# Kernel optimization log

Hardware: AMD Instinct MI355X
Metric: run time of the kernel (lower is better)

The kernel has to match this reference:

```python
import jax, jax.numpy as jnp
import numpy as np
import math

B, S, D_MODEL = 2, 2048, 1024
NUM_HEADS, D_KEY, D_VALUE = 16, 64, 64


def setup_inputs() -> dict:
    key = jax.random.key(0)
    ks = jax.random.split(key, 7)
    query = jax.random.normal(ks[0], (B, S, D_MODEL), dtype=jnp.float32)
    k_in = jax.random.normal(ks[1], (B, S, D_MODEL), dtype=jnp.float32)
    v_in = jax.random.normal(ks[2], (B, S, D_MODEL), dtype=jnp.float32)
    # boolean mask, True = masked out (masked_fill_ semantics); causal mask
    mask = jnp.triu(jnp.ones((S, S), dtype=bool), k=1)[None, None, :, :]
    scale = 1.0 / math.sqrt(D_MODEL)
    w_q = jax.random.normal(ks[3], (D_MODEL, NUM_HEADS * D_KEY), dtype=jnp.float32) * scale
    w_k = jax.random.normal(ks[4], (D_MODEL, NUM_HEADS * D_KEY), dtype=jnp.float32) * scale
    w_v = jax.random.normal(ks[5], (D_MODEL, NUM_HEADS * D_VALUE), dtype=jnp.float32) * scale
    w_o = jax.random.normal(ks[6], (NUM_HEADS * D_VALUE, D_MODEL), dtype=jnp.float32) * scale
    return {"query": query, "key": k_in, "value": v_in, "mask": mask,
            "w_q": w_q, "w_k": w_k, "w_v": w_v, "w_o": w_o}


def reference(query, key, value, mask, w_q, w_k, w_v, w_o):
    b, sq, _ = query.shape
    sk = key.shape[1]
    # projections, split heads: [B, H, S, d]
    q = (query @ w_q).reshape(b, sq, NUM_HEADS, D_KEY).transpose(0, 2, 1, 3)
    k = (key @ w_k).reshape(b, sk, NUM_HEADS, D_KEY).transpose(0, 2, 1, 3)
    v = (value @ w_v).reshape(b, sk, NUM_HEADS, D_VALUE).transpose(0, 2, 1, 3)
    # scaled scores [B, H, Sq, Sk], eager masked softmax (as in source)
    scores = jnp.einsum('bhqd,bhkd->bhqk', q, k) / math.sqrt(D_KEY)
    scores = jnp.where(mask, -jnp.inf, scores)
    attn = jax.nn.softmax(scores, axis=-1)
    # AV, merge heads, output projection (dropout is identity in eval / p=0)
    out = jnp.einsum('bhqk,bhkd->bhqd', attn, v)
    out = out.transpose(0, 2, 1, 3).reshape(b, sq, NUM_HEADS * D_VALUE)
    return out @ w_o
```

## Files before the change

### kernel.cpp

```cpp
#include <hip/hip_runtime.h>


typedef __attribute__((ext_vector_type(8))) short v8s;
typedef __attribute__((ext_vector_type(4))) float v4f;

#define MFMA16(a, b, c) __builtin_amdgcn_mfma_f32_16x16x32_bf16(a, b, c, 0, 0, 0)

#define GLOBAL_AS __attribute__((address_space(1)))
#define LDS_AS __attribute__((address_space(3)))

__device__ __forceinline__ void gload_lds16(const void* g, void* l) {
  __builtin_amdgcn_global_load_lds((const GLOBAL_AS void*)g, (LDS_AS void*)l, 16, 0, 0);
}

__device__ __forceinline__ short f2bf(float f) {
  union { float f; unsigned u; } x; x.f = f;
  unsigned r = x.u + 0x7fffu + ((x.u >> 16) & 1u);
  return (short)(r >> 16);
}

__device__ __forceinline__ unsigned cvtpk_bf16(float a, float b) {
  unsigned r;
  asm("v_cvt_pk_bf16_f32 %0, %1, %2" : "=v"(r) : "v"(a), "v"(b));
  return r;
}

__device__ __forceinline__ float exp2_hw(float x) {
  float r;
  asm("v_exp_f32 %0, %1" : "=v"(r) : "v"(x));
  return r;
}

__global__ __launch_bounds__(256) void wtrans_kernel(const float* __restrict__ w0,
                                                     const float* __restrict__ w1,
                                                     const float* __restrict__ w2,
                                                     const float* __restrict__ w3,
                                                     short* __restrict__ wtbase) {
  __shared__ __align__(16) short tile[64 * 72];
  const int NN = 1024;
  int z = blockIdx.z;
  const float* W = (z == 0) ? w0 : (z == 1) ? w1 : (z == 2) ? w2 : w3;
  short* Wt = wtbase + ((z < 3) ? ((size_t)(z + 1) << 20) : 0);
  float scale = (z == 0) ? 0.125f * 1.44269504f : 1.0f;
  int n0 = blockIdx.x * 64, k0 = blockIdx.y * 64;
  int t = threadIdx.x;
  int r = t >> 4;
  int c4 = (t & 15) * 4;
  for (int rr = r; rr < 64; rr += 16) {
    float4 f = *(const float4*)(W + (size_t)(k0 + rr) * NN + n0 + c4);
    tile[(c4 + 0) * 72 + rr] = f2bf(f.x * scale);
    tile[(c4 + 1) * 72 + rr] = f2bf(f.y * scale);
    tile[(c4 + 2) * 72 + rr] = f2bf(f.z * scale);
    tile[(c4 + 3) * 72 + rr] = f2bf(f.w * scale);
  }
  __syncthreads();
  int nr = t >> 2, kc = (t & 3) * 16;
  v8s v0 = *(const v8s*)&tile[nr * 72 + kc];
  v8s v1 = *(const v8s*)&tile[nr * 72 + kc + 8];
  *(v8s*)(Wt + (size_t)(n0 + nr) * NN + k0 + kc) = v0;
  *(v8s*)(Wt + (size_t)(n0 + nr) * NN + k0 + kc + 8) = v1;
}

__global__ __launch_bounds__(256) void cast3_kernel(const float* __restrict__ s0,
                                                    const float* __restrict__ s1,
                                                    const float* __restrict__ s2,
                                                    short* __restrict__ dst,
                                                    size_t zstride) {
  int z = blockIdx.z;
  const float* src = (z == 0) ? s0 : (z == 1) ? s1 : s2;
  short* d = dst + (size_t)z * zstride;
  int i = (blockIdx.x * 256 + threadIdx.x) * 8;
  float4 f0 = *(const float4*)(src + i);
  float4 f1 = *(const float4*)(src + i + 4);
  v8s v;
  v[0] = f2bf(f0.x); v[1] = f2bf(f0.y); v[2] = f2bf(f0.z); v[3] = f2bf(f0.w);
  v[4] = f2bf(f1.x); v[5] = f2bf(f1.y); v[6] = f2bf(f1.z); v[7] = f2bf(f1.w);
  *(v8s*)(d + i) = v;
}

template <bool OUT_F32, bool V_TRANS>
__global__ __launch_bounds__(256) void gemm2_kernel(
    const short* __restrict__ Ab, size_t sA,
    const short* __restrict__ Btb, size_t sB,
    short* __restrict__ Cb, float* __restrict__ Cf, size_t sC,
    short* __restrict__ Vt,
    int M, int N, int K) {
  __shared__ __align__(16) short As[2][128 * 32];
  __shared__ __align__(16) short Bs[2][128 * 32];

  int gx = gridDim.x, gy = gridDim.y;
  int id = blockIdx.x + gx * (blockIdx.y + gy * blockIdx.z);
  int nwg = gx * gy * gridDim.z;
  int v = (id & 7) * (nwg >> 3) + (id >> 3);
  int bx = v % gx;
  int by = (v / gx) % gy;
  int bz = v / (gx * gy);

  const short* A = Ab + (size_t)bz * sA;
  const short* Bt = Btb + (size_t)bz * sB;
  int row0 = by * 128, col0 = bx * 128;
  int t = threadIdx.x, lane = t & 63, w = t >> 6;
  int wm = (w >> 1) * 64, wn = (w & 1) * 64;
  int lr = lane & 15, lg = lane >> 4;

  v4f acc[4][4];
#pragma unroll
  for (int i = 0; i < 4; ++i)
#pragma unroll
    for (int j = 0; j < 4; ++j) acc[i][j] = {0.f, 0.f, 0.f, 0.f};

  int rl = lane >> 2, sl = lane & 3;
  int scol = ((sl ^ (rl ^ (rl >> 2))) & 3) * 8;
  const short* gA = A + (size_t)(row0 + w * 16 + rl) * K + scol;
  const short* gB = Bt + (size_t)(col0 + w * 16 + rl) * K + scol;
  const size_t rstep = (size_t)64 * K;

#define GEMM_STAGE(buf, k0_)                              \
  do {                                                    \
    gload_lds16(gA + (k0_), &As[buf][w * 512]);           \
    gload_lds16(gA + rstep + (k0_), &As[buf][(w + 4) * 512]); \
    gload_lds16(gB + (k0_), &Bs[buf][w * 512]);           \
    gload_lds16(gB + rstep + (k0_), &Bs[buf][(w + 4) * 512]); \
  } while (0)

  GEMM_STAGE(0, 0);
  __syncthreads();
  int cur = 0;
  int rsw = (lr ^ (lr >> 2)) & 3;
  for (int k0 = 0; k0 < K; k0 += 32) {
    if (k0 + 32 < K) GEMM_STAGE(cur ^ 1, k0 + 32);
    v8s af[4], bg[4];
#pragma unroll
    for (int mf = 0; mf < 4; ++mf)
      af[mf] = *(const v8s*)&As[cur][(wm + mf * 16 + lr) * 32 + ((lg ^ rsw) * 8)];
#pragma unroll
    for (int nf = 0; nf < 4; ++nf)
      bg[nf] = *(const v8s*)&Bs[cur][(wn + nf * 16 + lr) * 32 + ((lg ^ rsw) * 8)];
    __builtin_amdgcn_s_setprio(1);
#pragma unroll
    for (int mf = 0; mf < 4; ++mf)
#pragma unroll
      for (int nf = 0; nf < 4; ++nf)
        acc[mf][nf] = MFMA16(af[mf], bg[nf], acc[mf][nf]);
    __builtin_amdgcn_s_setprio(0);
    __syncthreads();
    cur ^= 1;
  }
#undef GEMM_STAGE

  if (V_TRANS && bz == 2) {
#pragma unroll
    for (int mf = 0; mf < 4; ++mf)
#pragma unroll
      for (int nf = 0; nf < 4; ++nf) {
        int col = col0 + wn + nf * 16 + lr;
        int row = row0 + wm + mf * 16 + lg * 4;
        int bh = ((row >> 11) << 4) + (col >> 6);
        int d = col & 63, s = row & 2047;
        uint2 u;
        u.x = cvtpk_bf16(acc[mf][nf][0], acc[mf][nf][1]);
        u.y = cvtpk_bf16(acc[mf][nf][2], acc[mf][nf][3]);
        *(uint2*)&Vt[((size_t)bh * 64 + d) * 2048 + s] = u;
      }
  } else {
#pragma unroll
    for (int mf = 0; mf < 4; ++mf)
#pragma unroll
      for (int nf = 0; nf < 4; ++nf)
#pragma unroll
        for (int r = 0; r < 4; ++r) {
          int row = row0 + wm + mf * 16 + lg * 4 + r;
          int col = col0 + wn + nf * 16 + lr;
          if (OUT_F32)
            (Cf + (size_t)bz * sC)[(size_t)row * N + col] = acc[mf][nf][r];
          else
            (Cb + (size_t)bz * sC)[(size_t)row * N + col] = f2bf(acc[mf][nf][r]);
        }
  }
}

__global__ __launch_bounds__(512, 4) void attn_kernel(const short* __restrict__ Qm,
                                                      const short* __restrict__ Km,
                                                      const short* __restrict__ Vt_g,
                                                      short* __restrict__ Cm) {
  const int S = 2048, DM = 1024;
  __shared__ __align__(16) short lds[21504];
  short* Ks0 = lds;
  short* Vs0 = lds + 8192;
  short* Pt = lds + 16384;
  v4f* scr = (v4f*)lds;

  int id = blockIdx.y * 16 + blockIdx.x;
  int v = (id & 7) * 64 + (id >> 3);
  int bh = v >> 4;
  int px = v & 15;
  int b = bh >> 4, h = bh & 15;
  int t = threadIdx.x, lane = t & 63, w = t >> 6;
  int g = w & 3, hh = w >> 2;
  int lr = lane & 15, lg = lane >> 4;
  size_t base = (size_t)b * S * DM + h * 64;
  size_t vbase = (size_t)bh * 64 * S;

  int srow = w * 8 + (lane >> 3);
  int scol = ((lane & 7) ^ (lane >> 3)) * 8;
  const short* gK = Km + base + (size_t)srow * DM + scol;
  const short* gV = Vt_g + vbase + (size_t)srow * S + scol;
  int sw = (lr & 7) * 8;

  const v8s vone = {0x3F80, 0x3F80, 0x3F80, 0x3F80,
                    0x3F80, 0x3F80, 0x3F80, 0x3F80};

#define ATTN_STAGE(buf, kt_)                                                  \
  do {                                                                        \
    size_t k0_ = (size_t)(kt_) * 64;                                          \
    gload_lds16(gK + k0_ * DM, &Ks0[(buf) * 4096 + w * 512]);                 \
    gload_lds16(gV + k0_, &Vs0[(buf) * 4096 + w * 512]);                      \
  } while (0)

  short* Cp = Cm + base;

#pragma unroll 1
  for (int qsel = 0; qsel < 2; ++qsel) {
    int qt = qsel ? px : (31 - px);
    int qbase = qt * 64 + g * 16;
    int qg = qbase + lr;
    int nkt = qt + 1;

    const short* Qp = Qm + base + (size_t)(qbase + lr) * DM + lg * 8;
    v8s q0 = *(const v8s*)Qp;
    v8s q1 = *(const v8s*)(Qp + 32);

    v4f o[5];
#pragma unroll
    for (int d4 = 0; d4 < 5; ++d4) o[d4] = {0.f, 0.f, 0.f, 0.f};

    ATTN_STAGE(0, 0);
    __syncthreads();
    int cur = 0;
#pragma unroll 1
    for (int kt = 0; kt < nkt; ++kt) {
      if (kt + 1 < nkt) ATTN_STAGE(cur ^ 1, kt + 1);
      int k0 = kt * 64;
      const short* Kc = &Ks0[cur * 4096];
      const short* Vc = &Vs0[cur * 4096];

      v8s ka0[2], ka1[2], vf[4];
#pragma unroll
      for (int t2 = 0; t2 < 2; ++t2) {
        int kr = hh * 32 + t2 * 16 + lr;
        ka0[t2] = *(const v8s*)&Kc[kr * 64 + ((lg * 8) ^ sw)];
        ka1[t2] = *(const v8s*)&Kc[kr * 64 + ((32 + lg * 8) ^ sw)];
      }
#pragma unroll
      for (int d4 = 0; d4 < 4; ++d4)
        vf[d4] = *(const v8s*)&Vc[(d4 * 16 + lr) * 64 + ((hh * 32 + lg * 8) ^ sw)];

      v4f st[2];
      __builtin_amdgcn_s_setprio(1);
#pragma unroll
      for (int t2 = 0; t2 < 2; ++t2) {
        v4f s = {0.f, 0.f, 0.f, 0.f};
        s = MFMA16(ka0[t2], q0, s);
        s = MFMA16(ka1[t2], q1, s);
        st[t2] = s;
      }
      __builtin_amdgcn_s_setprio(0);

      if (kt == nkt - 1) {
#pragma unroll
        for (int t2 = 0; t2 < 2; ++t2)
#pragma unroll
          for (int r = 0; r < 4; ++r)
            if (k0 + hh * 32 + t2 * 16 + lg * 4 + r > qg) st[t2][r] = -1e30f;
      }

#pragma unroll
      for (int t2 = 0; t2 < 2; ++t2) {
        uint2 u;
        u.x = cvtpk_bf16(exp2_hw(st[t2][0]), exp2_hw(st[t2][1]));
        u.y = cvtpk_bf16(exp2_hw(st[t2][2]), exp2_hw(st[t2][3]));
        *(uint2*)&Pt[w * 640 + lr * 40 + t2 * 16 + lg * 4] = u;
      }
      v8s pa = *(const v8s*)&Pt[w * 640 + lr * 40 + lg * 8];

      __builtin_amdgcn_s_setprio(1);
#pragma unroll
      for (int d4 = 0; d4 < 4; ++d4) o[d4] = MFMA16(pa, vf[d4], o[d4]);
      o[4] = MFMA16(pa, vone, o[4]);
      __builtin_amdgcn_s_setprio(0);
      __syncthreads();
      cur ^= 1;
    }

    if (hh == 1) {
#pragma unroll
      for (int d4 = 0; d4 < 5; ++d4) scr[(g * 5 + d4) * 64 + lane] = o[d4];
    }
    __syncthreads();
    if (hh == 0) {
#pragma unroll
      for (int d4 = 0; d4 < 5; ++d4) {
        v4f p = scr[(g * 5 + d4) * 64 + lane];
#pragma unroll
        for (int r = 0; r < 4; ++r) o[d4][r] += p[r];
      }
      float sv[4];
#pragma unroll
      for (int r = 0; r < 4; ++r) sv[r] = 1.0f / o[4][r];
#pragma unroll
      for (int r = 0; r < 4; ++r)
#pragma unroll
        for (int d4 = 0; d4 < 4; ++d4)
          Cp[(size_t)(qbase + lg * 4 + r) * DM + d4 * 16 + lr] =
              f2bf(o[d4][r] * sv[r]);
    }
    __syncthreads();
  }
#undef ATTN_STAGE
}

extern "C" void kernel_launch(void* const* d_in, const int* in_sizes, int n_in,
                              void* d_out, int out_size, void* d_ws, size_t ws_size,
                              hipStream_t stream) {
  const float* q_in = (const float*)d_in[0];
  const float* k_in = (const float*)d_in[1];
  const float* v_in = (const float*)d_in[2];
  const float* w_q = (const float*)d_in[4];
  const float* w_k = (const float*)d_in[5];
  const float* w_v = (const float*)d_in[6];
  const float* w_o = (const float*)d_in[7];
  float* outp = (float*)d_out;

  short* ws = (short*)d_ws;
  const size_t M1 = (size_t)1 << 20;
  short* Wto = ws;
  short* Wtq = ws + 1 * M1;
  short* X = ws + 4 * M1;
  short* Qb = ws + 16 * M1;
  short* Vtg = ws + 24 * M1;
  short* Cb = ws + 28 * M1;
  dim3 tb(256);
  dim3 tba(512);

  wtrans_kernel<<<dim3(16, 16, 4), tb, 0, stream>>>(w_q, w_k, w_v, w_o, ws);
  cast3_kernel<<<dim3(2048, 1, 3), tb, 0, stream>>>(q_in, k_in, v_in, X, 4 * M1);
  gemm2_kernel<false, true><<<dim3(8, 32, 3), tb, 0, stream>>>(
      X, 4 * M1, Wtq, M1, Qb, nullptr, 4 * M1, Vtg, 4096, 1024, 1024);
  attn_kernel<<<dim3(16, 32), tba, 0, stream>>>(Qb, Qb + 4 * M1, Vtg, Cb);
  gemm2_kernel<true, false><<<dim3(8, 32, 1), tb, 0, stream>>>(
      Cb, 0, Wto, 0, nullptr, outp, 0, nullptr, 4096, 1024, 1024);
}
```

Before: 112.3 us.

## Merge weight transpose and input cast kernels; use 64x128 GEMM tiles

Folds the weight transpose/cast and activation cast kernels into one launch, so there is one less kernel launch and the two memory-bound phases run together. The projection GEMMs move from 128x128 to 64x128 output tiles: four warps split N by 32 each, grids double, and launch bounds ask for 6 blocks per CU. This spreads the work over more workgroups on the many CUs, which should help with the small output-projection grid (256 blocks). The cost is lower arithmetic intensity per tile and more A/B reloads from global memory.

```diff
diff --git a/kernel.cpp b/kernel.cpp
--- a/kernel.cpp
+++ b/kernel.cpp
@@ -31,61 +31,65 @@
   return r;
 }
 
-__global__ __launch_bounds__(256) void wtrans_kernel(const float* __restrict__ w0,
-                                                     const float* __restrict__ w1,
-                                                     const float* __restrict__ w2,
-                                                     const float* __restrict__ w3,
-                                                     short* __restrict__ wtbase) {
+__global__ __launch_bounds__(256) void prep_kernel(const float* __restrict__ w0,
+                                                   const float* __restrict__ w1,
+                                                   const float* __restrict__ w2,
+                                                   const float* __restrict__ w3,
+                                                   short* __restrict__ wtbase,
+                                                   const float* __restrict__ s0,
+                                                   const float* __restrict__ s1,
+                                                   const float* __restrict__ s2,
+                                                   short* __restrict__ X,
+                                                   size_t xstride) {
   __shared__ __align__(16) short tile[64 * 72];
   const int NN = 1024;
-  int z = blockIdx.z;
-  const float* W = (z == 0) ? w0 : (z == 1) ? w1 : (z == 2) ? w2 : w3;
-  short* Wt = wtbase + ((z < 3) ? ((size_t)(z + 1) << 20) : 0);
-  float scale = (z == 0) ? 0.125f * 1.44269504f : 1.0f;
-  int n0 = blockIdx.x * 64, k0 = blockIdx.y * 64;
+  int bid = blockIdx.x;
   int t = threadIdx.x;
-  int r = t >> 4;
-  int c4 = (t & 15) * 4;
-  for (int rr = r; rr < 64; rr += 16) {
-    float4 f = *(const float4*)(W + (size_t)(k0 + rr) * NN + n0 + c4);
-    tile[(c4 + 0) * 72 + rr] = f2bf(f.x * scale);
-    tile[(c4 + 1) * 72 + rr] = f2bf(f.y * scale);
-    tile[(c4 + 2) * 72 + rr] = f2bf(f.z * scale);
-    tile[(c4 + 3) * 72 + rr] = f2bf(f.w * scale);
+  if (bid < 1024) {
+    int z = bid >> 8;
+    int rem = bid & 255;
+    int n0 = (rem & 15) * 64, k0 = (rem >> 4) * 64;
+    const float* W = (z == 0) ? w0 : (z == 1) ? w1 : (z == 2) ? w2 : w3;
+    short* Wt = wtbase + ((z < 3) ? ((size_t)(z + 1) << 20) : 0);
+    float scale = (z == 0) ? 0.125f * 1.44269504f : 1.0f;
+    int r = t >> 4;
+    int c4 = (t & 15) * 4;
+    for (int rr = r; rr < 64; rr += 16) {
+      float4 f = *(const float4*)(W + (size_t)(k0 + rr) * NN + n0 + c4);
+      tile[(c4 + 0) * 72 + rr] = f2bf(f.x * scale);
+      tile[(c4 + 1) * 72 + rr] = f2bf(f.y * scale);
+      tile[(c4 + 2) * 72 + rr] = f2bf(f.z * scale);
+      tile[(c4 + 3) * 72 + rr] = f2bf(f.w * scale);
+    }
+    __syncthreads();
+    int nr = t >> 2, kc = (t & 3) * 16;
+    v8s v0 = *(const v8s*)&tile[nr * 72 + kc];
+    v8s v1 = *(const v8s*)&tile[nr * 72 + kc + 8];
+    *(v8s*)(Wt + (size_t)(n0 + nr) * NN + k0 + kc) = v0;
+    *(v8s*)(Wt + (size_t)(n0 + nr) * NN + k0 + kc + 8) = v1;
+  } else {
+    int c = bid - 1024;
+    int z = c >> 11;
+    const float* src = (z == 0) ? s0 : (z == 1) ? s1 : s2;
+    short* d = X + (size_t)z * xstride;
+    int i = ((c & 2047) * 256 + t) * 8;
+    float4 f0 = *(const float4*)(src + i);
+    float4 f1 = *(const float4*)(src + i + 4);
+    v8s v;
+    v[0] = f2bf(f0.x); v[1] = f2bf(f0.y); v[2] = f2bf(f0.z); v[3] = f2bf(f0.w);
+    v[4] = f2bf(f1.x); v[5] = f2bf(f1.y); v[6] = f2bf(f1.z); v[7] = f2bf(f1.w);
+    *(v8s*)(d + i) = v;
   }
-  __syncthreads();
-  int nr = t >> 2, kc = (t & 3) * 16;
-  v8s v0 = *(const v8s*)&tile[nr * 72 + kc];
-  v8s v1 = *(const v8s*)&tile[nr * 72 + kc + 8];
-  *(v8s*)(Wt + (size_t)(n0 + nr) * NN + k0 + kc) = v0;
-  *(v8s*)(Wt + (size_t)(n0 + nr) * NN + k0 + kc + 8) = v1;
-}
-
-__global__ __launch_bounds__(256) void cast3_kernel(const float* __restrict__ s0,
-                                                    const float* __restrict__ s1,
-                                                    const float* __restrict__ s2,
-                                                    short* __restrict__ dst,
-                                                    size_t zstride) {
-  int z = blockIdx.z;
-  const float* src = (z == 0) ? s0 : (z == 1) ? s1 : s2;
-  short* d = dst + (size_t)z * zstride;
-  int i = (blockIdx.x * 256 + threadIdx.x) * 8;
-  float4 f0 = *(const float4*)(src + i);
-  float4 f1 = *(const float4*)(src + i + 4);
-  v8s v;
-  v[0] = f2bf(f0.x); v[1] = f2bf(f0.y); v[2] = f2bf(f0.z); v[3] = f2bf(f0.w);
-  v[4] = f2bf(f1.x); v[5] = f2bf(f1.y); v[6] = f2bf(f1.z); v[7] = f2bf(f1.w);
-  *(v8s*)(d + i) = v;
 }
 
 template <bool OUT_F32, bool V_TRANS>
-__global__ __launch_bounds__(256) void gemm2_kernel(
+__global__ __launch_bounds__(256, 6) void gemm64_kernel(
     const short* __restrict__ Ab, size_t sA,
     const short* __restrict__ Btb, size_t sB,
     short* __restrict__ Cb, float* __restrict__ Cf, size_t sC,
     short* __restrict__ Vt,
     int M, int N, int K) {
-  __shared__ __align__(16) short As[2][128 * 32];
+  __shared__ __align__(16) short As[2][64 * 32];
   __shared__ __align__(16) short Bs[2][128 * 32];
 
   int gx = gridDim.x, gy = gridDim.y;
@@ -98,16 +102,16 @@
 
   const short* A = Ab + (size_t)bz * sA;
   const short* Bt = Btb + (size_t)bz * sB;
-  int row0 = by * 128, col0 = bx * 128;
+  int row0 = by * 64, col0 = bx * 128;
   int t = threadIdx.x, lane = t & 63, w = t >> 6;
-  int wm = (w >> 1) * 64, wn = (w & 1) * 64;
+  int wn = w * 32;
   int lr = lane & 15, lg = lane >> 4;
 
-  v4f acc[4][4];
+  v4f acc[4][2];
 #pragma unroll
   for (int i = 0; i < 4; ++i)
 #pragma unroll
-    for (int j = 0; j < 4; ++j) acc[i][j] = {0.f, 0.f, 0.f, 0.f};
+    for (int j = 0; j < 2; ++j) acc[i][j] = {0.f, 0.f, 0.f, 0.f};
 
   int rl = lane >> 2, sl = lane & 3;
   int scol = ((sl ^ (rl ^ (rl >> 2))) & 3) * 8;
@@ -115,11 +119,10 @@
   const short* gB = Bt + (size_t)(col0 + w * 16 + rl) * K + scol;
   const size_t rstep = (size_t)64 * K;
 
-#define GEMM_STAGE(buf, k0_)                              \
-  do {                                                    \
-    gload_lds16(gA + (k0_), &As[buf][w * 512]);           \
-    gload_lds16(gA + rstep + (k0_), &As[buf][(w + 4) * 512]); \
-    gload_lds16(gB + (k0_), &Bs[buf][w * 512]);           \
+#define GEMM_STAGE(buf, k0_)                                  \
+  do {                                                        \
+    gload_lds16(gA + (k0_), &As[buf][w * 512]);               \
+    gload_lds16(gB + (k0_), &Bs[buf][w * 512]);               \
     gload_lds16(gB + rstep + (k0_), &Bs[buf][(w + 4) * 512]); \
   } while (0)
 
@@ -129,18 +132,18 @@
   int rsw = (lr ^ (lr >> 2)) & 3;
   for (int k0 = 0; k0 < K; k0 += 32) {
     if (k0 + 32 < K) GEMM_STAGE(cur ^ 1, k0 + 32);
-    v8s af[4], bg[4];
+    v8s af[4], bg[2];
 #pragma unroll
     for (int mf = 0; mf < 4; ++mf)
-      af[mf] = *(const v8s*)&As[cur][(wm + mf * 16 + lr) * 32 + ((lg ^ rsw) * 8)];
-#pragma unroll
-    for (int nf = 0; nf < 4; ++nf)
+      af[mf] = *(const v8s*)&As[cur][(mf * 16 + lr) * 32 + ((lg ^ rsw) * 8)];
+#pragma unroll
+    for (int nf = 0; nf < 2; ++nf)
       bg[nf] = *(const v8s*)&Bs[cur][(wn + nf * 16 + lr) * 32 + ((lg ^ rsw) * 8)];
     __builtin_amdgcn_s_setprio(1);
 #pragma unroll
     for (int mf = 0; mf < 4; ++mf)
 #pragma unroll
-      for (int nf = 0; nf < 4; ++nf)
+      for (int nf = 0; nf < 2; ++nf)
         acc[mf][nf] = MFMA16(af[mf], bg[nf], acc[mf][nf]);
     __builtin_amdgcn_s_setprio(0);
     __syncthreads();
@@ -152,9 +155,9 @@
 #pragma unroll
     for (int mf = 0; mf < 4; ++mf)
 #pragma unroll
-      for (int nf = 0; nf < 4; ++nf) {
+      for (int nf = 0; nf < 2; ++nf) {
         int col = col0 + wn + nf * 16 + lr;
-        int row = row0 + wm + mf * 16 + lg * 4;
+        int row = row0 + mf * 16 + lg * 4;
         int bh = ((row >> 11) << 4) + (col >> 6);
         int d = col & 63, s = row & 2047;
         uint2 u;
@@ -166,10 +169,10 @@
 #pragma unroll
     for (int mf = 0; mf < 4; ++mf)
 #pragma unroll
-      for (int nf = 0; nf < 4; ++nf)
+      for (int nf = 0; nf < 2; ++nf)
 #pragma unroll
         for (int r = 0; r < 4; ++r) {
-          int row = row0 + wm + mf * 16 + lg * 4 + r;
+          int row = row0 + mf * 16 + lg * 4 + r;
           int col = col0 + wn + nf * 16 + lr;
           if (OUT_F32)
             (Cf + (size_t)bz * sC)[(size_t)row * N + col] = acc[mf][nf][r];
@@ -342,11 +345,11 @@
   dim3 tb(256);
   dim3 tba(512);
 
-  wtrans_kernel<<<dim3(16, 16, 4), tb, 0, stream>>>(w_q, w_k, w_v, w_o, ws);
-  cast3_kernel<<<dim3(2048, 1, 3), tb, 0, stream>>>(q_in, k_in, v_in, X, 4 * M1);
-  gemm2_kernel<false, true><<<dim3(8, 32, 3), tb, 0, stream>>>(
+  prep_kernel<<<dim3(7168), tb, 0, stream>>>(w_q, w_k, w_v, w_o, ws,
+                                             q_in, k_in, v_in, X, 4 * M1);
+  gemm64_kernel<false, true><<<dim3(8, 64, 3), tb, 0, stream>>>(
       X, 4 * M1, Wtq, M1, Qb, nullptr, 4 * M1, Vtg, 4096, 1024, 1024);
   attn_kernel<<<dim3(16, 32), tba, 0, stream>>>(Qb, Qb + 4 * M1, Vtg, Cb);
-  gemm2_kernel<true, false><<<dim3(8, 32, 1), tb, 0, stream>>>(
+  gemm64_kernel<true, false><<<dim3(8, 64, 1), tb, 0, stream>>>(
       Cb, 0, Wto, 0, nullptr, outp, 0, nullptr, 4096, 1024, 1024);
 }
```

Measured after the change: 113.6 us. No clear change (+1.2%).
